# Kernel optimization log

Measured on AMD Instinct MI355X. Metric: run time of the kernel, lower is better.

## Reference

```python
import jax, jax.numpy as jnp
import numpy as np

S = 7       # grid size
B = 2       # boxes per cell
C = 20      # classes
IMG = 448.0 # image size
CELL = IMG / S
LAMBDA_COORD = 5.0
LAMBDA_NOOBJ = 0.5


def _iou(b1, b2):
    # b1, b2: [..., 4] corner boxes (x1, y1, x2, y2); broadcastable
    ix1 = jnp.maximum(b1[..., 0], b2[..., 0])
    iy1 = jnp.maximum(b1[..., 1], b2[..., 1])
    ix2 = jnp.minimum(b1[..., 2], b2[..., 2])
    iy2 = jnp.minimum(b1[..., 3], b2[..., 3])
    inter = jnp.clip(ix2 - ix1, 0.0) * jnp.clip(iy2 - iy1, 0.0)
    a1 = jnp.clip(b1[..., 2] - b1[..., 0], 0.0) * jnp.clip(b1[..., 3] - b1[..., 1], 0.0)
    a2 = jnp.clip(b2[..., 2] - b2[..., 0], 0.0) * jnp.clip(b2[..., 3] - b2[..., 1], 0.0)
    return inter / (a1 + a2 - inter + 1e-6)


def setup_inputs() -> dict:
    key = jax.random.key(0)
    k1, k2, k3, k4, k5, k6 = jax.random.split(key, 6)
    N, G = 16384, 8
    featmap = jax.random.uniform(k1, (N, S, S, 5 * B + C), dtype=jnp.float32)
    cx = jax.random.uniform(k2, (N, G), minval=32.0, maxval=416.0)
    cy = jax.random.uniform(k3, (N, G), minval=32.0, maxval=416.0)
    w = jax.random.uniform(k4, (N, G), minval=20.0, maxval=200.0)
    h = jax.random.uniform(k5, (N, G), minval=20.0, maxval=200.0)
    bboxes = jnp.stack([
        jnp.clip(cx - 0.5 * w, 0.0, IMG),
        jnp.clip(cy - 0.5 * h, 0.0, IMG),
        jnp.clip(cx + 0.5 * w, 0.0, IMG),
        jnp.clip(cy + 0.5 * h, 0.0, IMG),
    ], axis=-1).astype(jnp.float32)
    cls_labels = jax.random.randint(k6, (N, G), 0, C)
    return {"featmap": featmap, "bboxes": bboxes, "cls_labels": cls_labels}


def reference(featmap, bboxes, cls_labels):
    # featmap: [N, S, S, 5B+C] predictions; bboxes: [N, G, 4] GT corners; cls_labels: [N, G]
    N, _, _, D = featmap.shape
    G = bboxes.shape[1]
    x1g, y1g, x2g, y2g = bboxes[..., 0], bboxes[..., 1], bboxes[..., 2], bboxes[..., 3]
    cx = 0.5 * (x1g + x2g)
    cy = 0.5 * (y1g + y2g)
    gw = x2g - x1g
    gh = y2g - y1g
    # grid cell containing each GT center
    col = jnp.clip(jnp.floor(cx / CELL).astype(jnp.int32), 0, S - 1)
    row = jnp.clip(jnp.floor(cy / CELL).astype(jnp.int32), 0, S - 1)
    idx = row * S + col                                   # [N, G]
    flat = featmap.reshape(N, S * S, D)
    cell = jnp.take_along_axis(flat, jnp.broadcast_to(idx[:, :, None], (N, G, D)), axis=1)  # [N, G, D]
    boxp = cell[..., :5 * B].reshape(N, G, B, 5)
    px, py, pw, ph, pc = (boxp[..., i] for i in range(5))  # each [N, G, B]
    # predicted boxes in absolute image coords (x,y offsets within cell; w,h relative to image)
    gx0 = col.astype(featmap.dtype) * CELL
    gy0 = row.astype(featmap.dtype) * CELL
    pcx = gx0[..., None] + px * CELL
    pcy = gy0[..., None] + py * CELL
    pwa = pw * IMG
    pha = ph * IMG
    pred_box = jnp.stack([pcx - 0.5 * pwa, pcy - 0.5 * pha,
                          pcx + 0.5 * pwa, pcy + 0.5 * pha], axis=-1)  # [N, G, B, 4]
    iou = _iou(pred_box, bboxes[:, :, None, :])            # [N, G, B]
    resp = jax.nn.one_hot(jnp.argmax(iou, axis=-1), B, dtype=featmap.dtype)  # [N, G, B]
    tx = cx / CELL - col.astype(featmap.dtype)
    ty = cy / CELL - row.astype(featmap.dtype)
    tw = gw / IMG
    th = gh / IMG
    coord = ((px - tx[..., None]) ** 2 + (py - ty[..., None]) ** 2
             + (jnp.sqrt(jnp.clip(pw, 0.0)) - jnp.sqrt(tw)[..., None]) ** 2
             + (jnp.sqrt(jnp.clip(ph, 0.0)) - jnp.sqrt(th)[..., None]) ** 2)
    coord_loss = LAMBDA_COORD * jnp.sum(resp * coord)
    conf_obj = jnp.sum(resp * (pc - iou) ** 2)
    # noobj confidence loss over every predictor, minus the responsible ones
    conf_all = featmap[..., jnp.arange(B) * 5 + 4]          # [N, S, S, B]
    noobj = LAMBDA_NOOBJ * (jnp.sum(conf_all ** 2) - jnp.sum(resp * pc ** 2))
    clsp = cell[..., 5 * B:]                                # [N, G, C]
    cls_loss = jnp.sum((clsp - jax.nn.one_hot(cls_labels, C, dtype=featmap.dtype)) ** 2)
    return jnp.reshape(coord_loss + conf_obj + noobj + cls_loss, (1,))
```

## Files before the change

kernel.cpp:

```cpp
#include <hip/hip_runtime.h>

#define D_CH 30
#define CELL_SZ 64.0f
#define INV_CELL (1.0f / 64.0f)
#define INV_IMG (1.0f / 448.0f)
#define IMG_SZ 448.0f
#define L_COORD 5.0f
#define L_NOOBJ 0.5f

#define CONF_BLOCKS 2048
#define BLK 256
#define STRIDE4 ((unsigned)CONF_BLOCKS * (unsigned)BLK)
#define DCH1 ((unsigned)(((unsigned long long)STRIDE4 * 4ull) % 30ull))
#define DCH4 ((unsigned)(((unsigned long long)STRIDE4 * 16ull) % 30ull))

__device__ __forceinline__ float wave_reduce(float v) {
#pragma unroll
    for (int o = 32; o > 0; o >>= 1) v += __shfl_down(v, o, 64);
    return v;
}

__device__ __forceinline__ float pick_conf_sq(float4 v, unsigned ch) {
    float p = 0.0f;
    p = (ch == 2u) ? v.z : p;
    p = (ch == 4u) ? v.x : p;
    p = (ch == 6u) ? v.w : p;
    p = (ch == 8u) ? v.y : p;
    return p * p;
}

__global__ __launch_bounds__(BLK) void yolo_loss_kernel(
    const float* __restrict__ fm, const float* __restrict__ bb,
    const int* __restrict__ lab, float* __restrict__ out,
    unsigned total , int ng, int G)
{
    float acc = 0.0f;

    if (blockIdx.x < CONF_BLOCKS) {
        const float4* __restrict__ fm4 = (const float4*)fm;
        const unsigned total4 = total >> 2;
        unsigned i = blockIdx.x * BLK + threadIdx.x;
        unsigned ch = (4u * i) % 30u;
        float cacc = 0.0f;

        while (i + 3u * STRIDE4 < total4) {
            float4 v0 = fm4[i];
            float4 v1 = fm4[i + STRIDE4];
            float4 v2 = fm4[i + 2u * STRIDE4];
            float4 v3 = fm4[i + 3u * STRIDE4];
            unsigned c1 = ch + DCH1; if (c1 >= 30u) c1 -= 30u;
            unsigned c2 = c1 + DCH1; if (c2 >= 30u) c2 -= 30u;
            unsigned c3 = c2 + DCH1; if (c3 >= 30u) c3 -= 30u;
            cacc += pick_conf_sq(v0, ch);
            cacc += pick_conf_sq(v1, c1);
            cacc += pick_conf_sq(v2, c2);
            cacc += pick_conf_sq(v3, c3);
            ch += DCH4; if (ch >= 30u) ch -= 30u;
            i += 4u * STRIDE4;
        }
        for (; i < total4; i += STRIDE4) {
            float4 v = fm4[i];
            cacc += pick_conf_sq(v, (4u * i) % 30u);
        }
        if (blockIdx.x == 0 && threadIdx.x == 0) {
            for (unsigned f = total4 << 2; f < total; ++f) {
                unsigned c = f % 30u;
                if (c == 4u || c == 9u) { float e = fm[f]; cacc += e * e; }
            }
        }
        acc = L_NOOBJ * cacc;
    } else {
        int t = (blockIdx.x - CONF_BLOCKS) * BLK + threadIdx.x;
        if (t < ng) {
            float4 box = ((const float4*)bb)[t];
            float x1 = box.x, y1 = box.y, x2 = box.z, y2 = box.w;
            float cx = 0.5f * (x1 + x2);
            float cy = 0.5f * (y1 + y2);
            float gw = x2 - x1, gh = y2 - y1;
            int col = (int)floorf(cx * INV_CELL); col = min(max(col, 0), 6);
            int row = (int)floorf(cy * INV_CELL); row = min(max(row, 0), 6);

            const float* __restrict__ cell =
                fm + ((size_t)(t / G) * 49 + (size_t)(row * 7 + col)) * D_CH;
            const float2* __restrict__ c2 = (const float2*)cell;
            float2 u0 = c2[0];
            float2 u1 = c2[1];
            float2 u2 = c2[2];
            float2 u3 = c2[3];
            float2 u4 = c2[4];

            float tx = cx * INV_CELL - (float)col;
            float ty = cy * INV_CELL - (float)row;
            float stw = sqrtf(gw * INV_IMG);
            float sth = sqrtf(gh * INV_IMG);
            float ga = fmaxf(gw, 0.0f) * fmaxf(gh, 0.0f);

            float px[2] = {u0.x, u2.y};
            float py[2] = {u0.y, u3.x};
            float pw[2] = {u1.x, u3.y};
            float ph[2] = {u1.y, u4.x};
            float pc[2] = {u2.x, u4.y};

            float ioub[2], coordb[2];
#pragma unroll
            for (int b = 0; b < 2; ++b) {
                float pcx = ((float)col + px[b]) * CELL_SZ;
                float pcy = ((float)row + py[b]) * CELL_SZ;
                float pwa = pw[b] * IMG_SZ, pha = ph[b] * IMG_SZ;
                float bx1 = pcx - 0.5f * pwa, by1 = pcy - 0.5f * pha;
                float bx2 = pcx + 0.5f * pwa, by2 = pcy + 0.5f * pha;
                float ix1 = fmaxf(bx1, x1), iy1 = fmaxf(by1, y1);
                float ix2 = fminf(bx2, x2), iy2 = fminf(by2, y2);
                float inter = fmaxf(ix2 - ix1, 0.0f) * fmaxf(iy2 - iy1, 0.0f);
                float a1 = fmaxf(bx2 - bx1, 0.0f) * fmaxf(by2 - by1, 0.0f);
                ioub[b] = inter / (a1 + ga - inter + 1e-6f);
                float dx = px[b] - tx, dy = py[b] - ty;
                float dw = sqrtf(fmaxf(pw[b], 0.0f)) - stw;
                float dh = sqrtf(fmaxf(ph[b], 0.0f)) - sth;
                coordb[b] = dx * dx + dy * dy + dw * dw + dh * dh;
            }
            int sel = (ioub[1] > ioub[0]) ? 1 : 0;
            acc += L_COORD * coordb[sel];
            float dpc = pc[sel] - ioub[sel];
            acc += dpc * dpc;
            acc -= L_NOOBJ * pc[sel] * pc[sel];

            float sq = 0.0f;
#pragma unroll
            for (int k = 0; k < 10; ++k) {
                float2 u = c2[5 + k];
                sq = fmaf(u.x, u.x, fmaf(u.y, u.y, sq));
            }
            float cl = cell[10 + lab[t]];
            acc += sq - 2.0f * cl + 1.0f;
        }
    }

    __shared__ float sm[4];
    float wv = wave_reduce(acc);
    int lane = threadIdx.x & 63;
    int wid = threadIdx.x >> 6;
    if (lane == 0) sm[wid] = wv;
    __syncthreads();
    if (threadIdx.x == 0) {
        float s = sm[0] + sm[1] + sm[2] + sm[3];
        atomicAdd(out, s);
    }
}

extern "C" void kernel_launch(void* const* d_in, const int* in_sizes, int n_in,
                              void* d_out, int out_size, void* d_ws, size_t ws_size,
                              hipStream_t stream) {
    const float* fm = (const float*)d_in[0];
    const float* bb = (const float*)d_in[1];
    const int* lab = (const int*)d_in[2];
    float* out = (float*)d_out;

    int fm_elems = in_sizes[0];
    int ng = in_sizes[2];
    int n = fm_elems / (49 * D_CH);
    int G = ng / n;
    unsigned total = (unsigned)n * 49u * (unsigned)D_CH;

    hipMemsetAsync(out, 0, sizeof(float), stream);

    const int ng_blocks = (ng + BLK - 1) / BLK;
    yolo_loss_kernel<<<CONF_BLOCKS + ng_blocks, BLK, 0, stream>>>(
        fm, bb, lab, out, total, ng, G);
}
```

Measured before the change: 161.1 us.

## Fuse GT and confidence work per block with last-block partial reduction

New measurement: 279.2 us. 1.73x slower.

```diff
diff --git a/kernel.cpp b/kernel.cpp
--- a/kernel.cpp
+++ b/kernel.cpp
@@ -8,9 +8,9 @@
 #define L_COORD 5.0f
 #define L_NOOBJ 0.5f
 
-#define CONF_BLOCKS 2048
 #define BLK 256
-#define STRIDE4 ((unsigned)CONF_BLOCKS * (unsigned)BLK)
+#define GRID 2048
+#define STRIDE4 ((unsigned)GRID * (unsigned)BLK)
 #define DCH1 ((unsigned)(((unsigned long long)STRIDE4 * 4ull) % 30ull))
 #define DCH4 ((unsigned)(((unsigned long long)STRIDE4 * 16ull) % 30ull))
 
@@ -29,49 +29,17 @@
     return p * p;
 }
 
-__global__ __launch_bounds__(BLK) void yolo_loss_kernel(
+__global__ __launch_bounds__(BLK) void yolo_fused_kernel(
     const float* __restrict__ fm, const float* __restrict__ bb,
     const int* __restrict__ lab, float* __restrict__ out,
-    unsigned total , int ng, int G)
+    float* __restrict__ partials, unsigned* __restrict__ counter,
+    unsigned total , int ng, int G, int items_per_block)
 {
     float acc = 0.0f;
 
-    if (blockIdx.x < CONF_BLOCKS) {
-        const float4* __restrict__ fm4 = (const float4*)fm;
-        const unsigned total4 = total >> 2;
-        unsigned i = blockIdx.x * BLK + threadIdx.x;
-        unsigned ch = (4u * i) % 30u;
-        float cacc = 0.0f;
-
-        while (i + 3u * STRIDE4 < total4) {
-            float4 v0 = fm4[i];
-            float4 v1 = fm4[i + STRIDE4];
-            float4 v2 = fm4[i + 2u * STRIDE4];
-            float4 v3 = fm4[i + 3u * STRIDE4];
-            unsigned c1 = ch + DCH1; if (c1 >= 30u) c1 -= 30u;
-            unsigned c2 = c1 + DCH1; if (c2 >= 30u) c2 -= 30u;
-            unsigned c3 = c2 + DCH1; if (c3 >= 30u) c3 -= 30u;
-            cacc += pick_conf_sq(v0, ch);
-            cacc += pick_conf_sq(v1, c1);
-            cacc += pick_conf_sq(v2, c2);
-            cacc += pick_conf_sq(v3, c3);
-            ch += DCH4; if (ch >= 30u) ch -= 30u;
-            i += 4u * STRIDE4;
-        }
-        for (; i < total4; i += STRIDE4) {
-            float4 v = fm4[i];
-            cacc += pick_conf_sq(v, (4u * i) % 30u);
-        }
-        if (blockIdx.x == 0 && threadIdx.x == 0) {
-            for (unsigned f = total4 << 2; f < total; ++f) {
-                unsigned c = f % 30u;
-                if (c == 4u || c == 9u) { float e = fm[f]; cacc += e * e; }
-            }
-        }
-        acc = L_NOOBJ * cacc;
-    } else {
-        int t = (blockIdx.x - CONF_BLOCKS) * BLK + threadIdx.x;
-        if (t < ng) {
+    {
+        int t = (int)blockIdx.x * items_per_block + (int)threadIdx.x;
+        if ((int)threadIdx.x < items_per_block && t < ng) {
             float4 box = ((const float4*)bb)[t];
             float x1 = box.x, y1 = box.y, x2 = box.z, y2 = box.w;
             float cx = 0.5f * (x1 + x2);
@@ -136,15 +104,67 @@
         }
     }
 
+    {
+        const float4* __restrict__ fm4 = (const float4*)fm;
+        const unsigned total4 = total >> 2;
+        unsigned i = blockIdx.x * BLK + threadIdx.x;
+        unsigned ch = (4u * i) % 30u;
+        float cacc = 0.0f;
+
+        while (i + 3u * STRIDE4 < total4) {
+            float4 v0 = fm4[i];
+            float4 v1 = fm4[i + STRIDE4];
+            float4 v2 = fm4[i + 2u * STRIDE4];
+            float4 v3 = fm4[i + 3u * STRIDE4];
+            unsigned c1 = ch + DCH1; if (c1 >= 30u) c1 -= 30u;
+            unsigned c2 = c1 + DCH1; if (c2 >= 30u) c2 -= 30u;
+            unsigned c3 = c2 + DCH1; if (c3 >= 30u) c3 -= 30u;
+            cacc += pick_conf_sq(v0, ch);
+            cacc += pick_conf_sq(v1, c1);
+            cacc += pick_conf_sq(v2, c2);
+            cacc += pick_conf_sq(v3, c3);
+            ch += DCH4; if (ch >= 30u) ch -= 30u;
+            i += 4u * STRIDE4;
+        }
+        for (; i < total4; i += STRIDE4) {
+            float4 v = fm4[i];
+            cacc += pick_conf_sq(v, (4u * i) % 30u);
+        }
+        if (blockIdx.x == 0 && threadIdx.x == 0) {
+            for (unsigned f = total4 << 2; f < total; ++f) {
+                unsigned c = f % 30u;
+                if (c == 4u || c == 9u) { float e = fm[f]; cacc += e * e; }
+            }
+        }
+        acc += L_NOOBJ * cacc;
+    }
+
     __shared__ float sm[4];
+    __shared__ int is_last;
     float wv = wave_reduce(acc);
     int lane = threadIdx.x & 63;
     int wid = threadIdx.x >> 6;
     if (lane == 0) sm[wid] = wv;
     __syncthreads();
     if (threadIdx.x == 0) {
-        float s = sm[0] + sm[1] + sm[2] + sm[3];
-        atomicAdd(out, s);
+        float bsum = sm[0] + sm[1] + sm[2] + sm[3];
+        __hip_atomic_store(&partials[blockIdx.x], bsum,
+                           __ATOMIC_RELEASE, __HIP_MEMORY_SCOPE_AGENT);
+        unsigned prev = __hip_atomic_fetch_add(counter, 1u,
+                           __ATOMIC_ACQ_REL, __HIP_MEMORY_SCOPE_AGENT);
+        is_last = (prev == gridDim.x - 1u) ? 1 : 0;
+    }
+    __syncthreads();
+
+    if (is_last) {
+        float a = 0.0f;
+        for (unsigned i = threadIdx.x; i < gridDim.x; i += BLK)
+            a += __hip_atomic_load(&partials[i],
+                     __ATOMIC_RELAXED, __HIP_MEMORY_SCOPE_AGENT);
+        float w2 = wave_reduce(a);
+        if (lane == 0) sm[wid] = w2;
+        __syncthreads();
+        if (threadIdx.x == 0) out[0] = sm[0] + sm[1] + sm[2] + sm[3];
     }
 }
 
@@ -156,15 +176,17 @@
     const int* lab = (const int*)d_in[2];
     float* out = (float*)d_out;
 
+    unsigned* counter = (unsigned*)d_ws;
+    float* partials = (float*)d_ws + 64;
+
     int fm_elems = in_sizes[0];
     int ng = in_sizes[2];
     int n = fm_elems / (49 * D_CH);
     int G = ng / n;
     unsigned total = (unsigned)n * 49u * (unsigned)D_CH;
+    int items_per_block = (ng + GRID - 1) / GRID;
 
-    hipMemsetAsync(out, 0, sizeof(float), stream);
-
-    const int ng_blocks = (ng + BLK - 1) / BLK;
-    yolo_loss_kernel<<<CONF_BLOCKS + ng_blocks, BLK, 0, stream>>>(
-        fm, bb, lab, out, total, ng, G);
+    hipMemsetAsync(counter, 0, sizeof(unsigned), stream);
+    yolo_fused_kernel<<<GRID, BLK, 0, stream>>>(
+        fm, bb, lab, out, partials, counter, total, ng, G, items_per_block);
 }
```
